# Kernel optimization log

Measured on AMD Instinct MI355X. Metric: run time of the kernel, lower is better.

Reference implementation:

```python
import jax, jax.numpy as jnp
import numpy as np

N_EMBD = 1024
N_HEAD = 16
B, L = 2, 2048


def setup_inputs() -> dict:
    key = jax.random.key(0)
    k1, k2, k3, k4 = jax.random.split(key, 4)
    x = jax.random.normal(k1, (B, L, N_EMBD), dtype=jnp.float32)
    W_qkv = jax.random.normal(k2, (N_EMBD, 3 * N_EMBD), dtype=jnp.float32) * 0.02
    b_qkv = jnp.zeros((3 * N_EMBD,), dtype=jnp.float32)
    W_o = jax.random.normal(k3, (N_EMBD, N_EMBD), dtype=jnp.float32) * 0.02
    b_o = jnp.zeros((N_EMBD,), dtype=jnp.float32)
    mask_len = jax.random.randint(k4, (B,), 1, L, dtype=jnp.int32)
    return {"x": x, "W_qkv": W_qkv, "b_qkv": b_qkv, "W_o": W_o, "b_o": b_o,
            "mask_len": mask_len}


def reference(x, W_qkv, b_qkv, W_o, b_o, mask_len):
    Bx, Lx, E = x.shape
    H = N_HEAD
    D = E // H
    # causal mask [1,1,L,L]; then zero out query rows i >= mask_len[b]
    mask = jnp.tri(Lx)[None, None, :, :]
    row_invalid = jnp.arange(Lx).reshape(1, 1, Lx, 1) >= mask_len.reshape(Bx, 1, 1, 1)
    mask = jnp.where(row_invalid, 0.0, mask)  # [B,1,L,L]
    # QKV projection; note original packs per-head 3D-chunks: reshape (B,L,H,3D)
    h = x @ W_qkv + b_qkv                      # [B,L,3E]
    h = h.reshape(Bx, Lx, H, 3 * D).transpose(0, 2, 1, 3)  # [B,H,L,3D]
    q, k, v = jnp.split(h, 3, axis=-1)         # each [B,H,L,D]
    attn = jnp.einsum('bhqd,bhkd->bhqk', q, k) / jnp.sqrt(jnp.float32(D))
    attn = jnp.where(mask == 0, -1e18, attn)
    attn = jax.nn.softmax(attn, axis=-1)
    # dropout: deterministic (train=False) -> identity
    y = jnp.einsum('bhqk,bhkd->bhqd', attn, v)  # [B,H,L,D]
    y = y.transpose(0, 2, 1, 3).reshape(Bx, Lx, E)
    return y @ W_o + b_o
```

## Files before the change

### kernel.cpp

```cpp
#include <hip/hip_runtime.h>

typedef unsigned short u16;
typedef unsigned int u32;
typedef __bf16 bf16x8 __attribute__((ext_vector_type(8)));
typedef float f32x4 __attribute__((ext_vector_type(4)));
typedef u16 u16x4 __attribute__((ext_vector_type(4)));
typedef u16 u16x8 __attribute__((ext_vector_type(8)));

#define LSEQ 2048
#define EMB  1024
#define NH   16
#define HDIM 64

#define QSCALE 0.1803368808f

#if __has_builtin(__builtin_amdgcn_exp2f)
#define EXP2(x) __builtin_amdgcn_exp2f(x)
#else
#define EXP2(x) __expf((x) * 0.6931471805599453f)
#endif

__device__ __forceinline__ u16 cvt_bf(float f) {
  __bf16 h = (__bf16)f;
  return __builtin_bit_cast(u16, h);
}
__device__ __forceinline__ float bf2f(u16 v) {
  return __uint_as_float(((unsigned)v) << 16);
}
__device__ __forceinline__ void async16(void* lds, const void* g) {
  __builtin_amdgcn_global_load_lds((const __attribute__((address_space(1))) void*)g,
                                   (__attribute__((address_space(3))) void*)lds, 16, 0, 0);
}
__device__ __forceinline__ f32x4 mfma16(bf16x8 a, bf16x8 b, f32x4 c) {
  return __builtin_amdgcn_mfma_f32_16x16x32_bf16(a, b, c, 0, 0, 0);
}

__global__ void prep(const float* __restrict__ x, u16* __restrict__ xb,
                     const float* __restrict__ Wqkv, u16* __restrict__ WqkvT,
                     const float* __restrict__ Wo, u16* __restrict__ WoT) {
  __shared__ float tile[32][33];
  const int bid = blockIdx.x;
  const int tid = threadIdx.x;
  if (bid < 2048) {
    const int n4 = 1024 * 1024;
    for (int i = bid * 256 + tid; i < n4; i += 2048 * 256) {
      float4 v = ((const float4*)x)[i];
      u16x4 o = { cvt_bf(v.x), cvt_bf(v.y), cvt_bf(v.z), cvt_bf(v.w) };
      ((u16x4*)xb)[i] = o;
    }
    return;
  }
  const int idx = bid - 2048;
  const int bx = idx & 127, by = idx >> 7;
  const int Kd = 1024;
  const float* in;
  u16* out;
  int Nd, n0;
  if (bx < 96) { in = Wqkv; out = WqkvT; Nd = 3072; n0 = bx * 32; }
  else         { in = Wo;   out = WoT;   Nd = 1024; n0 = (bx - 96) * 32; }
  const int k0 = by * 32;
  const int tx = tid & 31, ty = tid >> 5;
#pragma unroll
  for (int i = 0; i < 4; ++i)
    tile[ty + i * 8][tx] = in[(size_t)(k0 + ty + i * 8) * Nd + n0 + tx];
  __syncthreads();
#pragma unroll
  for (int i = 0; i < 4; ++i)
    out[(size_t)(n0 + ty + i * 8) * Kd + k0 + tx] = cvt_bf(tile[tx][ty + i * 8]);
}

template<int NCOLS, int MODE, int BM>
__launch_bounds__(256)
__global__ void gemm_bt(const u16* __restrict__ A, const u16* __restrict__ Bt,
                        const float* __restrict__ bias, float* __restrict__ Out,
                        u16* __restrict__ Qo, u16* __restrict__ Ko, u16* __restrict__ Vo,
                        const int* __restrict__ mask_len) {
  constexpr int MF = BM / 32;
  constexpr int ABUF = BM * 32;
  __shared__ __attribute__((aligned(16))) u16 SMEM[3 * ABUF + 3 * 128 * 32];
  u16* As = SMEM;
  u16* Bs = SMEM + 3 * ABUF;
  const int tid = threadIdx.x;
  const int w = tid >> 6, l = tid & 63;
  const int g = l >> 4, cc = l & 15;
  constexpr int GX = NCOLS / 128;
  constexpr int NWG = (4096 / BM) * GX;
  constexpr int CPX = NWG / 8;
  const int orig = blockIdx.y * GX + blockIdx.x;
  const int wgid = (orig & 7) * CPX + (orig >> 3);
  const int m0 = (wgid / GX) * BM, n0 = (wgid % GX) * 128;
  const int wm = w >> 1, wn = w & 1;
  const int K = 1024;

  int type = 0, tbh = 0;
  if constexpr (MODE == 0) {
    const int tb = wgid % GX;
    type = tb >> 3;
    tbh = tb & 7;
    const int bb = m0 >> 11;
    if (type < 2 && (m0 & (LSEQ - 1)) >= mask_len[bb]) return;
  }

  const int srow = tid >> 2;
  const int scol = (tid & 3) * 8;
  const u16* Ag = A + (size_t)(m0 + srow) * K + scol;
  const u16 *Bg0, *Bg1;
  if constexpr (MODE == 0) {
    Bg0 = Bt + (size_t)((2 * tbh) * 192 + type * 64 + srow) * K + scol;
    Bg1 = Bt + (size_t)((2 * tbh + 1) * 192 + type * 64 + srow) * K + scol;
  } else {
    Bg0 = Bt + (size_t)(n0 + srow) * K + scol;
    Bg1 = Bt + (size_t)(n0 + srow + 64) * K + scol;
  }
  f32x4 acc[MF][4] = {};

  auto stage = [&](int buf, int k0) {
    async16(&As[buf * ABUF + w * 512], Ag + k0);
    if constexpr (BM == 128)
      async16(&As[buf * ABUF + 2048 + w * 512], Ag + (size_t)64 * K + k0);
    async16(&Bs[buf * 4096 + w * 512], Bg0 + k0);
    async16(&Bs[buf * 4096 + 2048 + w * 512], Bg1 + k0);
  };

  stage(0, 0);
  stage(1, 32);
  int buf = 0;
  for (int k0 = 0; k0 < K; k0 += 32) {
    if (k0 + 32 < K) {
      if constexpr (BM == 128) asm volatile("s_waitcnt vmcnt(4)" ::: "memory");
      else                     asm volatile("s_waitcnt vmcnt(3)" ::: "memory");
    } else {
      asm volatile("s_waitcnt vmcnt(0)" ::: "memory");
    }
    __builtin_amdgcn_s_barrier();
    __builtin_amdgcn_sched_barrier(0);
    if (k0 + 64 < K) {
      int nb = buf + 2; if (nb >= 3) nb -= 3;
      stage(nb, k0 + 64);
    }
    bf16x8 af[MF], bfr[4];
#pragma unroll
    for (int mf = 0; mf < MF; ++mf)
      af[mf] = *(const bf16x8*)&As[buf * ABUF + (wm * (BM / 2) + mf * 16 + cc) * 32 + g * 8];
#pragma unroll
    for (int nf = 0; nf < 4; ++nf)
      bfr[nf] = *(const bf16x8*)&Bs[buf * 4096 + (wn * 64 + nf * 16 + cc) * 32 + g * 8];
#pragma unroll
    for (int mf = 0; mf < MF; ++mf)
#pragma unroll
      for (int nf = 0; nf < 4; ++nf)
        acc[mf][nf] = mfma16(af[mf], bfr[nf], acc[mf][nf]);
    if (++buf == 3) buf = 0;
  }

  if constexpr (MODE == 0) {
    __syncthreads();
    char* pane0 = (char*)SMEM;
    char* pane1 = (char*)(SMEM + 3 * ABUF);
    const int bb = m0 >> 11;
    {
      const int hw = 2 * tbh + wn;
      const float* bptr = bias + hw * 192 + type * 64;
      char* P = wn ? pane1 : pane0;
#pragma unroll
      for (int mf = 0; mf < MF; ++mf) {
#pragma unroll
        for (int nf = 0; nf < 4; ++nf) {
          int d = nf * 16 + cc;
          float bv = bptr[d];
#pragma unroll
          for (int r = 0; r < 4; ++r) {
            int ml = wm * 64 + mf * 16 + g * 4 + r;
            float val = acc[mf][nf][r] + bv;
            if (type == 0) val *= QSCALE;
            u16 h = cvt_bf(val);
            if (type == 2) {
              int off = (ml * 2) & 127;
              *(u16*)(P + d * 256 + ((ml & 64) << 1) + (off ^ ((d & 7) << 4))) = h;
            } else {
              *(u16*)(P + ml * 128 + ((d * 2) ^ ((ml & 7) << 4))) = h;
            }
          }
        }
      }
    }
    __syncthreads();
#pragma unroll
    for (int wi = 0; wi < 2; ++wi) {
      const int head = 2 * tbh + wi;
      const int bh = bb * NH + head;
      const int ls0 = m0 & (LSEQ - 1);
      char* P = wi ? pane1 : pane0;
      if (type == 2) {
        u16* dstb = Vo + (size_t)bh * HDIM * LSEQ + ls0;
#pragma unroll
        for (int it = 0; it < 4; ++it) {
          int idx = it * 256 + tid;
          int row = idx >> 4;
          int colB = (idx & 15) * 16;
          int4 v = *(const int4*)(P + row * 256 + (colB & 128) + ((colB & 112) ^ ((row & 7) << 4)));
          *(int4*)((char*)(dstb + (size_t)row * LSEQ) + colB) = v;
        }
      } else {
        u16* dst = (type == 0 ? Qo : Ko) + ((size_t)bh * LSEQ + ls0) * HDIM;
#pragma unroll
        for (int it = 0; it < 4; ++it) {
          int idx = it * 256 + tid;
          int row = idx >> 3;
          int colB = (idx & 7) * 16;
          int4 v = *(const int4*)(P + row * 128 + (colB ^ ((row & 7) << 4)));
          *(int4*)((char*)dst + row * 128 + colB) = v;
        }
      }
    }
  } else {
#pragma unroll
    for (int mf = 0; mf < MF; ++mf) {
#pragma unroll
      for (int nf = 0; nf < 4; ++nf) {
        int n = n0 + wn * 64 + nf * 16 + cc;
        float bv = bias[n];
#pragma unroll
        for (int r = 0; r < 4; ++r) {
          int m = m0 + wm * (BM / 2) + mf * 16 + g * 4 + r;
          Out[(size_t)m * NCOLS + n] = acc[mf][nf][r] + bv;
        }
      }
    }
  }
}

__launch_bounds__(256)
__global__ void attn_fwd(const u16* __restrict__ Q, const u16* __restrict__ Kb,
                         const u16* __restrict__ Vt, const int* __restrict__ mask_len,
                         u16* __restrict__ Y) {
  __shared__ __attribute__((aligned(16))) u16 Ks[2][64 * 64];
  __shared__ __attribute__((aligned(16))) u16 Vs[2][64 * 64];
  __shared__ __attribute__((aligned(16))) u16 Ps[4 * 16 * 64];
  const int tid = threadIdx.x;
  const int i = blockIdx.x;

  if (i >= 1024) {
    float* partial = (float*)Ks;
    u16* mv = (u16*)((char*)Ks + 1024);
    int bh = i - 1024, b = bh >> 4, h = bh & (NH - 1);
    int d = tid >> 2, part = tid & 3;
    const u16* src = Vt + ((size_t)bh * HDIM + d) * LSEQ + part * 512;
    float s = 0.f;
    for (int ii = 0; ii < 512; ii += 8) {
      u16x8 v = *(const u16x8*)&src[ii];
#pragma unroll
      for (int jj = 0; jj < 8; ++jj) s += bf2f(v[jj]);
    }
    partial[tid] = s;
    __syncthreads();
    if (part == 0) {
      float t = partial[tid] + partial[tid + 1] + partial[tid + 2] + partial[tid + 3];
      mv[d] = cvt_bf(t * (1.0f / (float)LSEQ));
    }
    __syncthreads();
    int lo = mask_len[b];
    if (lo < 0) lo = 0;
    if (lo > LSEQ) lo = LSEQ;
    int total = (LSEQ - lo) * HDIM;
    for (int idx = tid; idx < total; idx += 256) {
      int row = lo + (idx >> 6), dd = idx & 63;
      Y[((size_t)b * LSEQ + row) * EMB + h * HDIM + dd] = mv[dd];
    }
    return;
  }

  const int w = tid >> 6, l = tid & 63;
  const int g = l >> 4, cc = l & 15;
  const int bh = i & 31;
  const int k = i >> 5, grp = k >> 3, j = k & 7;
  int qblk;
  if (grp == 0) qblk = 31 - j;
  else if (grp == 1) qblk = j;
  else if (grp == 2) qblk = 23 - j;
  else qblk = 8 + j;
  const int q0 = qblk * 64;
  const int nt = qblk + 1;
  const int b = bh >> 4, h = bh & (NH - 1);

  const int lo = mask_len[b];
  if (q0 >= lo) return;

  const int sr = w * 8 + (l >> 3);
  const int pb = (l & 7) * 16;
  char* Pw = (char*)&Ps[w * 16 * 64];
  const int xc = (cc & 7) << 4;

  auto stageKV = [&](int buf, int t) {
    const int kv0 = t * 64;
#pragma unroll
    for (int ch = 0; ch < 2; ++ch) {
      int R = sr + ch * 32;
      int dcol = (pb ^ ((R & 7) << 4)) >> 1;
      async16((char*)Ks[buf] + ch * 4096 + w * 1024,
              Kb + ((size_t)bh * LSEQ + kv0 + R) * HDIM + dcol);
      async16((char*)Vs[buf] + ch * 4096 + w * 1024,
              Vt + ((size_t)bh * HDIM + R) * LSEQ + kv0 + dcol);
    }
  };

  const u16* Qg = Q + ((size_t)bh * LSEQ + q0 + w * 16) * HDIM;
  bf16x8 qf0 = *(const bf16x8*)&Qg[cc * HDIM + g * 8];
  bf16x8 qf1 = *(const bf16x8*)&Qg[cc * HDIM + 32 + g * 8];

  bf16x8 onesf;
#pragma unroll
  for (int z = 0; z < 8; ++z) onesf[z] = (__bf16)1.0f;

  f32x4 o[4] = {};
  f32x4 ls = {};

  stageKV(0, 0);

  for (int t = 0; t < nt; ++t) {
    const int cur = t & 1;
    if (t + 1 < nt) {
      stageKV(cur ^ 1, t + 1);
      asm volatile("s_waitcnt vmcnt(4)" ::: "memory");
    } else {
      asm volatile("s_waitcnt vmcnt(0)" ::: "memory");
    }
    __builtin_amdgcn_s_barrier();
    __builtin_amdgcn_sched_barrier(0);
    const char* KsB = (const char*)Ks[cur];
    const char* VsB = (const char*)Vs[cur];

    f32x4 sf[4] = {};
    __builtin_amdgcn_s_setprio(1);
#pragma unroll
    for (int nf = 0; nf < 4; ++nf) {
      bf16x8 kf0 = *(const bf16x8*)(KsB + (nf * 16 + cc) * 128 + ((g * 16) ^ xc));
      bf16x8 kf1 = *(const bf16x8*)(KsB + (nf * 16 + cc) * 128 + ((64 + g * 16) ^ xc));
      sf[nf] = mfma16(qf0, kf0, sf[nf]);
      sf[nf] = mfma16(qf1, kf1, sf[nf]);
    }
    __builtin_amdgcn_s_setprio(0);

    if (t == nt - 1) {
#pragma unroll
      for (int nf = 0; nf < 4; ++nf) {
        int kvl = nf * 16 + cc;
#pragma unroll
        for (int r = 0; r < 4; ++r)
          if (kvl > w * 16 + g * 4 + r) sf[nf][r] = -1e30f;
      }
    }

#pragma unroll
    for (int r = 0; r < 4; ++r) {
      int q = g * 4 + r;
      int xr = (q & 7) << 4;
#pragma unroll
      for (int nf = 0; nf < 4; ++nf) {
        float pv = EXP2(sf[nf][r]);
        *(u16*)(Pw + q * 128 + (((nf * 16 + cc) * 2) ^ xr)) = cvt_bf(pv);
      }
    }
    asm volatile("s_waitcnt lgkmcnt(0)" ::: "memory");
    __builtin_amdgcn_sched_barrier(0);

    bf16x8 pf0 = *(const bf16x8*)(Pw + cc * 128 + ((g * 16) ^ xc));
    bf16x8 pf1 = *(const bf16x8*)(Pw + cc * 128 + ((64 + g * 16) ^ xc));
    __builtin_amdgcn_s_setprio(1);
    ls = mfma16(pf1, onesf, mfma16(pf0, onesf, ls));
#pragma unroll
    for (int nf = 0; nf < 4; ++nf) {
      bf16x8 vf0 = *(const bf16x8*)(VsB + (nf * 16 + cc) * 128 + ((g * 16) ^ xc));
      bf16x8 vf1 = *(const bf16x8*)(VsB + (nf * 16 + cc) * 128 + ((64 + g * 16) ^ xc));
      o[nf] = mfma16(pf0, vf0, o[nf]);
      o[nf] = mfma16(pf1, vf1, o[nf]);
    }
    __builtin_amdgcn_s_setprio(0);
    __builtin_amdgcn_s_barrier();
  }

#pragma unroll
  for (int r = 0; r < 4; ++r) {
    int row = q0 + w * 16 + g * 4 + r;
    if (row < lo) {
      float inv = 1.0f / ls[r];
      size_t base = ((size_t)b * LSEQ + row) * EMB + h * HDIM;
#pragma unroll
      for (int nf = 0; nf < 4; ++nf)
        Y[base + nf * 16 + cc] = cvt_bf(o[nf][r] * inv);
    }
  }
}

extern "C" void kernel_launch(void* const* d_in, const int* in_sizes, int n_in,
                              void* d_out, int out_size, void* d_ws, size_t ws_size,
                              hipStream_t stream) {
  (void)in_sizes; (void)n_in; (void)out_size; (void)ws_size;
  const float* x    = (const float*)d_in[0];
  const float* Wqkv = (const float*)d_in[1];
  const float* bqkv = (const float*)d_in[2];
  const float* Wo   = (const float*)d_in[3];
  const float* bo   = (const float*)d_in[4];
  const int* mask_len = (const int*)d_in[5];
  float* out = (float*)d_out;

  u16* ws = (u16*)d_ws;
  u16* xb    = ws;
  u16* wqkvt = ws + (size_t)4 * 1024 * 1024;
  u16* wot   = wqkvt + (size_t)3 * 1024 * 1024;
  u16* Qb    = wot + (size_t)1024 * 1024;
  u16* Kb    = Qb + (size_t)4 * 1024 * 1024;
  u16* Vtb   = Kb + (size_t)4 * 1024 * 1024;
  u16* Yb    = xb;

  prep<<<6144, 256, 0, stream>>>(x, xb, Wqkv, wqkvt, Wo, wot);
  gemm_bt<3072, 0, 128><<<dim3(24, 32), 256, 0, stream>>>(xb, wqkvt, bqkv, nullptr, Qb, Kb, Vtb, mask_len);
  attn_fwd<<<1056, 256, 0, stream>>>(Qb, Kb, Vtb, mask_len, Yb);
  gemm_bt<1024, 1, 64><<<dim3(8, 64), 256, 0, stream>>>(Yb, wot, bo, out, nullptr, nullptr, nullptr, nullptr);
}
```

Measured before the change: 98.97 us.

## Split QKV GEMM into dedicated kernel with K=64 tiles and swizzled LDS

Replaces the templated QKV projection with a dedicated kernel that stages K=64 slices into double-buffered, XOR-swizzled shared memory using four 16-byte async loads per operand per thread. Each tile now runs two MFMA k-steps per barrier. The kernel requests two workgroups per CU through launch bounds, and the epilogue swizzle patterns are changed. The aim is fewer barriers per unit of work, fewer LDS bank conflicts, and more occupancy, at the cost of more shared memory per block (64KB) and a second barrier per iteration.

```diff
diff --git a/kernel.cpp b/kernel.cpp
--- a/kernel.cpp
+++ b/kernel.cpp
@@ -69,12 +69,135 @@
     out[(size_t)(n0 + ty + i * 8) * Kd + k0 + tx] = cvt_bf(tile[tx][ty + i * 8]);
 }
 
-template<int NCOLS, int MODE, int BM>
+__launch_bounds__(256, 2)
+__global__ void gemm_qkv(const u16* __restrict__ A, const u16* __restrict__ Bt,
+                         const float* __restrict__ bias,
+                         u16* __restrict__ Qo, u16* __restrict__ Ko, u16* __restrict__ Vo,
+                         const int* __restrict__ mask_len) {
+  __shared__ __attribute__((aligned(16))) u16 SMEM[4 * 8192];
+  u16* As = SMEM;
+  u16* Bs = SMEM + 2 * 8192;
+  const int tid = threadIdx.x;
+  const int w = tid >> 6, l = tid & 63;
+  const int g = l >> 4, cc = l & 15;
+  const int orig = blockIdx.y * 24 + blockIdx.x;
+  const int wgid = (orig & 7) * 96 + (orig >> 3);
+  const int m0 = (wgid / 24) * 128;
+  const int tb = wgid % 24;
+  const int type = tb >> 3, tbh = tb & 7;
+  const int bb = m0 >> 11;
+  const int lo = mask_len[bb];
+  if (type < 2 && (m0 & (LSEQ - 1)) >= lo) return;
+  const int wm = w >> 1, wn = w & 1;
+  const int K = 1024;
+
+  const int srow8 = tid >> 3;
+  const int chunk = tid & 7;
+  auto stage = [&](int buf, int k0) {
+#pragma unroll
+    for (int c = 0; c < 4; ++c) {
+      int R = c * 32 + srow8;
+      int col = (chunk ^ (R & 7)) * 8;
+      async16((char*)&As[buf * 8192] + c * 4096 + w * 1024,
+              A + (size_t)(m0 + R) * K + k0 + col);
+      int gR = (2 * tbh + (R >> 6)) * 192 + type * 64 + (R & 63);
+      async16((char*)&Bs[buf * 8192] + c * 4096 + w * 1024,
+              Bt + (size_t)gR * K + k0 + col);
+    }
+  };
+
+  f32x4 acc[4][4] = {};
+  stage(0, 0);
+  for (int t = 0; t < 16; ++t) {
+    const int cur = t & 1;
+    if (t + 1 < 16) {
+      stage(cur ^ 1, (t + 1) * 64);
+      asm volatile("s_waitcnt vmcnt(8)" ::: "memory");
+    } else {
+      asm volatile("s_waitcnt vmcnt(0)" ::: "memory");
+    }
+    __builtin_amdgcn_s_barrier();
+    __builtin_amdgcn_sched_barrier(0);
+    const char* AB = (const char*)&As[cur * 8192];
+    const char* BB = (const char*)&Bs[cur * 8192];
+#pragma unroll
+    for (int ks = 0; ks < 2; ++ks) {
+      bf16x8 af[4], bfr[4];
+#pragma unroll
+      for (int mf = 0; mf < 4; ++mf) {
+        int row = wm * 64 + mf * 16 + cc;
+        af[mf] = *(const bf16x8*)(AB + row * 128 + ((ks * 64 + g * 16) ^ ((row & 7) << 4)));
+      }
+#pragma unroll
+      for (int nf = 0; nf < 4; ++nf) {
+        int row = wn * 64 + nf * 16 + cc;
+        bfr[nf] = *(const bf16x8*)(BB + row * 128 + ((ks * 64 + g * 16) ^ ((row & 7) << 4)));
+      }
+#pragma unroll
+      for (int mf = 0; mf < 4; ++mf)
+#pragma unroll
+        for (int nf = 0; nf < 4; ++nf)
+          acc[mf][nf] = mfma16(af[mf], bfr[nf], acc[mf][nf]);
+    }
+    __builtin_amdgcn_s_barrier();
+  }
+
+  __syncthreads();
+  {
+    char* P = (char*)SMEM + wn * 16384;
+    const float* bptr = bias + (2 * tbh + wn) * 192 + type * 64;
+#pragma unroll
+    for (int mf = 0; mf < 4; ++mf) {
+#pragma unroll
+      for (int nf = 0; nf < 4; ++nf) {
+        int d = nf * 16 + cc;
+        float bv = bptr[d];
+#pragma unroll
+        for (int r = 0; r < 4; ++r) {
+          int ml = wm * 64 + mf * 16 + g * 4 + r;
+          float val = acc[mf][nf][r] + bv;
+          if (type == 0) val *= QSCALE;
+          u16 hv = cvt_bf(val);
+          if (type == 2) *(u16*)(P + d * 256 + ((ml * 2) ^ ((d & 7) << 5))) = hv;
+          else           *(u16*)(P + ml * 128 + ((d * 2) ^ (((ml >> 2) & 3) << 5))) = hv;
+        }
+      }
+    }
+  }
+  __syncthreads();
+  const int ls0 = m0 & (LSEQ - 1);
+#pragma unroll
+  for (int wi = 0; wi < 2; ++wi) {
+    const int bh = bb * NH + 2 * tbh + wi;
+    char* P = (char*)SMEM + wi * 16384;
+    if (type == 2) {
+      u16* dstb = Vo + (size_t)bh * HDIM * LSEQ + ls0;
+#pragma unroll
+      for (int it = 0; it < 4; ++it) {
+        int idx = it * 256 + tid;
+        int row = idx >> 4;
+        int colB = (idx & 15) * 16;
+        int4 v = *(const int4*)(P + row * 256 + (colB ^ ((row & 7) << 5)));
+        *(int4*)((char*)(dstb + (size_t)row * LSEQ) + colB) = v;
+      }
+    } else {
+      u16* dst = (type == 0 ? Qo : Ko) + ((size_t)bh * LSEQ + ls0) * HDIM;
+#pragma unroll
+      for (int it = 0; it < 4; ++it) {
+        int idx = it * 256 + tid;
+        int row = idx >> 3;
+        int colB = (idx & 7) * 16;
+        int4 v = *(const int4*)(P + row * 128 + (colB ^ (((row >> 2) & 3) << 5)));
+        *(int4*)((char*)dst + row * 128 + colB) = v;
+      }
+    }
+  }
+}
+
+template<int NCOLS, int BM>
 __launch_bounds__(256)
-__global__ void gemm_bt(const u16* __restrict__ A, const u16* __restrict__ Bt,
-                        const float* __restrict__ bias, float* __restrict__ Out,
-                        u16* __restrict__ Qo, u16* __restrict__ Ko, u16* __restrict__ Vo,
-                        const int* __restrict__ mask_len) {
+__global__ void gemm_out(const u16* __restrict__ A, const u16* __restrict__ Bt,
+                         const float* __restrict__ bias, float* __restrict__ Out) {
   constexpr int MF = BM / 32;
   constexpr int ABUF = BM * 32;
   __shared__ __attribute__((aligned(16))) u16 SMEM[3 * ABUF + 3 * 128 * 32];
@@ -91,33 +214,15 @@
   const int m0 = (wgid / GX) * BM, n0 = (wgid % GX) * 128;
   const int wm = w >> 1, wn = w & 1;
   const int K = 1024;
-
-  int type = 0, tbh = 0;
-  if constexpr (MODE == 0) {
-    const int tb = wgid % GX;
-    type = tb >> 3;
-    tbh = tb & 7;
-    const int bb = m0 >> 11;
-    if (type < 2 && (m0 & (LSEQ - 1)) >= mask_len[bb]) return;
-  }
-
   const int srow = tid >> 2;
   const int scol = (tid & 3) * 8;
   const u16* Ag = A + (size_t)(m0 + srow) * K + scol;
-  const u16 *Bg0, *Bg1;
-  if constexpr (MODE == 0) {
-    Bg0 = Bt + (size_t)((2 * tbh) * 192 + type * 64 + srow) * K + scol;
-    Bg1 = Bt + (size_t)((2 * tbh + 1) * 192 + type * 64 + srow) * K + scol;
-  } else {
-    Bg0 = Bt + (size_t)(n0 + srow) * K + scol;
-    Bg1 = Bt + (size_t)(n0 + srow + 64) * K + scol;
-  }
+  const u16* Bg0 = Bt + (size_t)(n0 + srow) * K + scol;
+  const u16* Bg1 = Bt + (size_t)(n0 + srow + 64) * K + scol;
   f32x4 acc[MF][4] = {};
 
   auto stage = [&](int buf, int k0) {
     async16(&As[buf * ABUF + w * 512], Ag + k0);
-    if constexpr (BM == 128)
-      async16(&As[buf * ABUF + 2048 + w * 512], Ag + (size_t)64 * K + k0);
     async16(&Bs[buf * 4096 + w * 512], Bg0 + k0);
     async16(&Bs[buf * 4096 + 2048 + w * 512], Bg1 + k0);
   };
@@ -126,12 +231,8 @@
   stage(1, 32);
   int buf = 0;
   for (int k0 = 0; k0 < K; k0 += 32) {
-    if (k0 + 32 < K) {
-      if constexpr (BM == 128) asm volatile("s_waitcnt vmcnt(4)" ::: "memory");
-      else                     asm volatile("s_waitcnt vmcnt(3)" ::: "memory");
-    } else {
-      asm volatile("s_waitcnt vmcnt(0)" ::: "memory");
-    }
+    if (k0 + 32 < K) asm volatile("s_waitcnt vmcnt(3)" ::: "memory");
+    else             asm volatile("s_waitcnt vmcnt(0)" ::: "memory");
     __builtin_amdgcn_s_barrier();
     __builtin_amdgcn_sched_barrier(0);
     if (k0 + 64 < K) {
@@ -153,78 +254,16 @@
     if (++buf == 3) buf = 0;
   }
 
-  if constexpr (MODE == 0) {
-    __syncthreads();
-    char* pane0 = (char*)SMEM;
-    char* pane1 = (char*)(SMEM + 3 * ABUF);
-    const int bb = m0 >> 11;
-    {
-      const int hw = 2 * tbh + wn;
-      const float* bptr = bias + hw * 192 + type * 64;
-      char* P = wn ? pane1 : pane0;
-#pragma unroll
-      for (int mf = 0; mf < MF; ++mf) {
-#pragma unroll
-        for (int nf = 0; nf < 4; ++nf) {
-          int d = nf * 16 + cc;
-          float bv = bptr[d];
-#pragma unroll
-          for (int r = 0; r < 4; ++r) {
-            int ml = wm * 64 + mf * 16 + g * 4 + r;
-            float val = acc[mf][nf][r] + bv;
-            if (type == 0) val *= QSCALE;
-            u16 h = cvt_bf(val);
-            if (type == 2) {
-              int off = (ml * 2) & 127;
-              *(u16*)(P + d * 256 + ((ml & 64) << 1) + (off ^ ((d & 7) << 4))) = h;
-            } else {
-              *(u16*)(P + ml * 128 + ((d * 2) ^ ((ml & 7) << 4))) = h;
-            }
-          }
-        }
-      }
-    }
-    __syncthreads();
-#pragma unroll
-    for (int wi = 0; wi < 2; ++wi) {
-      const int head = 2 * tbh + wi;
-      const int bh = bb * NH + head;
-      const int ls0 = m0 & (LSEQ - 1);
-      char* P = wi ? pane1 : pane0;
-      if (type == 2) {
-        u16* dstb = Vo + (size_t)bh * HDIM * LSEQ + ls0;
-#pragma unroll
-        for (int it = 0; it < 4; ++it) {
-          int idx = it * 256 + tid;
-          int row = idx >> 4;
-          int colB = (idx & 15) * 16;
-          int4 v = *(const int4*)(P + row * 256 + (colB & 128) + ((colB & 112) ^ ((row & 7) << 4)));
-          *(int4*)((char*)(dstb + (size_t)row * LSEQ) + colB) = v;
-        }
-      } else {
-        u16* dst = (type == 0 ? Qo : Ko) + ((size_t)bh * LSEQ + ls0) * HDIM;
-#pragma unroll
-        for (int it = 0; it < 4; ++it) {
-          int idx = it * 256 + tid;
-          int row = idx >> 3;
-          int colB = (idx & 7) * 16;
-          int4 v = *(const int4*)(P + row * 128 + (colB ^ ((row & 7) << 4)));
-          *(int4*)((char*)dst + row * 128 + colB) = v;
-        }
-      }
-    }
-  } else {
-#pragma unroll
-    for (int mf = 0; mf < MF; ++mf) {
-#pragma unroll
-      for (int nf = 0; nf < 4; ++nf) {
-        int n = n0 + wn * 64 + nf * 16 + cc;
-        float bv = bias[n];
-#pragma unroll
-        for (int r = 0; r < 4; ++r) {
-          int m = m0 + wm * (BM / 2) + mf * 16 + g * 4 + r;
-          Out[(size_t)m * NCOLS + n] = acc[mf][nf][r] + bv;
-        }
+#pragma unroll
+  for (int mf = 0; mf < MF; ++mf) {
+#pragma unroll
+    for (int nf = 0; nf < 4; ++nf) {
+      int n = n0 + wn * 64 + nf * 16 + cc;
+      float bv = bias[n];
+#pragma unroll
+      for (int r = 0; r < 4; ++r) {
+        int m = m0 + wm * (BM / 2) + mf * 16 + g * 4 + r;
+        Out[(size_t)m * NCOLS + n] = acc[mf][nf][r] + bv;
       }
     }
   }
@@ -414,7 +453,7 @@
   u16* Yb    = xb;
 
   prep<<<6144, 256, 0, stream>>>(x, xb, Wqkv, wqkvt, Wo, wot);
-  gemm_bt<3072, 0, 128><<<dim3(24, 32), 256, 0, stream>>>(xb, wqkvt, bqkv, nullptr, Qb, Kb, Vtb, mask_len);
+  gemm_qkv<<<dim3(24, 32), 256, 0, stream>>>(xb, wqkvt, bqkv, Qb, Kb, Vtb, mask_len);
   attn_fwd<<<1056, 256, 0, stream>>>(Qb, Kb, Vtb, mask_len, Yb);
-  gemm_bt<1024, 1, 64><<<dim3(8, 64), 256, 0, stream>>>(Yb, wot, bo, out, nullptr, nullptr, nullptr, nullptr);
-}
+  gemm_out<1024, 64><<<dim3(8, 64), 256, 0, stream>>>(Yb, wot, bo, out);
+}
```

Result: faster. 94.40 us (-4.6%).
